# Performance work log

Measured on AMD Instinct MI355X. Metric: run time of the kernel, lower is better.

The kernel has to match this reference:

```python
import jax, jax.numpy as jnp
import numpy as np

EPS = 1e-8
N_CLASSES = 11


def _instance_loss(views_1, views_2, masks, labels):
    # views_*: [1, C, H, W]; masks: [1, K, H, W] binary; labels: [1, K] in [0,11)
    C = views_1.shape[1]
    X1 = views_1[0].reshape(C, -1)                      # [C, P]
    X2 = views_2[0].reshape(C, -1)                      # [C, P]
    K = masks.shape[1]
    M = (masks[0].reshape(K, -1) == 1).astype(X1.dtype) # [K, P]
    lab = labels[0]                                     # [K]

    counts = M.sum(axis=1)                              # [K] pixels per instance
    cnt = jnp.maximum(counts, 1.0)

    # per-instance mean feature vector over masked view-1 pixels
    per_chan_sum = M @ X1.T                             # [K, C]
    means = per_chan_sum / cnt[:, None]                 # [K, C]

    # torch.std over ALL elements of the gathered [N_k, C] block (unbiased)
    n_elem = counts * C                                 # [K]
    sum_all = per_chan_sum.sum(axis=1)                  # [K]
    mean_all = sum_all / jnp.maximum(n_elem, 1.0)
    sumsq = M @ (X1 * X1).sum(axis=0)                   # [K]
    var = (sumsq - n_elem * mean_all * mean_all) / jnp.maximum(n_elem - 1.0, 1.0)
    std = jnp.sqrt(jnp.maximum(var, 0.0))               # [K]

    # pairwise mean cosine sim: sim[i,j] = mean_{p in mask_j} cos(means[i], X2[:,p])
    norm_m = jnp.sqrt((means * means).sum(axis=1))      # [K]
    norm_2 = jnp.sqrt((X2 * X2).sum(axis=0))            # [P]
    D = means @ X2                                      # [K, P]
    ratio = D / jnp.maximum(norm_m[:, None] * norm_2[None, :], EPS)
    sim = (ratio @ M.T) / cnt[None, :]                  # [K, K]

    same = lab[:, None] == lab[None, :]
    eye = jnp.eye(K, dtype=bool)

    instance_sim = jnp.zeros(N_CLASSES, X1.dtype).at[lab].add(jnp.diagonal(sim))
    class_sim = jnp.zeros(N_CLASSES, X1.dtype).at[lab].add(
        jnp.where(same & ~eye, sim, 0.0).sum(axis=1))
    class_std = jnp.zeros(N_CLASSES, X1.dtype).at[lab].add(std)

    # negative-pair buckets: human={1,2}, 4wheel={3..8}, 2wheel={9,10}
    g_hum_4w = (lab >= 1) & (lab <= 8)                  # human or 4wheel
    g_4w_2w = (lab >= 3) & (lab <= 10)                  # 4wheel or 2wheel
    g_hum_2w = ((lab >= 1) & (lab <= 2)) | ((lab >= 9) & (lab <= 10))
    diff = ~same

    def neg_bucket(g):
        pair = diff & g[:, None] & g[None, :]
        c = pair.sum().astype(X1.dtype)
        s = jnp.where(pair, sim, 0.0).sum()
        return jnp.where(c > 1, s / c, s).reshape(1)

    neg_4w_hum = neg_bucket(g_hum_4w)
    neg_4w_2w = neg_bucket(g_4w_2w)
    neg_hum_2w = neg_bucket(g_hum_2w)

    class_counts = jnp.zeros(N_CLASSES, X1.dtype).at[lab].add(1.0)
    many = class_counts > 1
    instance_sim = jnp.where(many, instance_sim / jnp.maximum(class_counts, 1.0), instance_sim)
    class_sim = jnp.where(
        many, class_sim / jnp.maximum(class_counts * (class_counts - 1.0), 1.0), class_sim)
    class_std = jnp.where(many, class_std / jnp.maximum(class_counts, 1.0), class_std)

    return instance_sim, class_sim, neg_4w_hum, neg_4w_2w, neg_hum_2w, class_std


def setup_inputs() -> dict:
    key = jax.random.key(0)
    k1, k2, k3, k4 = jax.random.split(key, 4)
    views_1 = jax.random.normal(k1, (1, 64, 512, 512), dtype=jnp.float32)
    views_2 = jax.random.normal(k2, (1, 64, 512, 512), dtype=jnp.float32)
    masks = jax.random.randint(k3, (1, 16, 512, 512), 0, 2, dtype=jnp.int32)
    labels = jax.random.randint(k4, (1, 16), 0, 11, dtype=jnp.int32)
    return {"views_1": views_1, "views_2": views_2, "masks": masks, "labels": labels}


def reference(views_1, views_2, masks, labels):
    return _instance_loss(views_1, views_2, masks, labels)
```

## Files before the change

kernel.cpp:

```cpp
#include <hip/hip_runtime.h>

#define PIX 262144
#define CCH 64
#define KK  16

typedef __attribute__((ext_vector_type(8))) short short8;
typedef __attribute__((ext_vector_type(4))) float f32x4;

__device__ __forceinline__ float wred64(float v) {
    #pragma unroll
    for (int o = 32; o > 0; o >>= 1) v += __shfl_xor(v, o, 64);
    return v;
}

__global__ __launch_bounds__(256) void k2_all(
        const float* __restrict__ x1, const float* __restrict__ x2,
        const int* __restrict__ masks, float* __restrict__ counts_s,
        float* __restrict__ psum_c, float* __restrict__ psumsq_c,
        float* __restrict__ G_c) {
    __shared__ float gl[4][1024];
    int lane = threadIdx.x & 63;
    int wv   = threadIdx.x >> 6;
    int quad = lane >> 4;
    int n    = lane & 15;
    const short ONE = (short)0x3F80;
    const int* Mrow = masks + (size_t)n * PIX;

    if (blockIdx.x < 1024) {
        int b = blockIdx.x;
        int base = b * 256;
        int cp   = b & 31;
        const float* Xrow = x1 + (size_t)(wv * 16 + n) * PIX;

        f32x4 acc0 = {0.f, 0.f, 0.f, 0.f};
        f32x4 acc1 = {0.f, 0.f, 0.f, 0.f};
        int cnt = 0;

        for (int sc = 0; sc < 2; ++sc) {
            int4 mk[8]; float4 xa[4], xb[4];
            #pragma unroll
            for (int i = 0; i < 4; ++i) {
                int kof = base + sc * 128 + i * 32 + (quad << 3);
                mk[2*i]   = *(const int4*)(Mrow + kof);
                mk[2*i+1] = *(const int4*)(Mrow + kof + 4);
                xa[i] = *(const float4*)(Xrow + kof);
                xb[i] = *(const float4*)(Xrow + kof + 4);
            }
            #pragma unroll
            for (int i = 0; i < 4; ++i) {
                short8 af;
                af[0] = (mk[2*i].x   == 1) ? ONE : (short)0;
                af[1] = (mk[2*i].y   == 1) ? ONE : (short)0;
                af[2] = (mk[2*i].z   == 1) ? ONE : (short)0;
                af[3] = (mk[2*i].w   == 1) ? ONE : (short)0;
                af[4] = (mk[2*i+1].x == 1) ? ONE : (short)0;
                af[5] = (mk[2*i+1].y == 1) ? ONE : (short)0;
                af[6] = (mk[2*i+1].z == 1) ? ONE : (short)0;
                af[7] = (mk[2*i+1].w == 1) ? ONE : (short)0;
                cnt += (mk[2*i].x == 1) + (mk[2*i].y == 1) + (mk[2*i].z == 1) + (mk[2*i].w == 1)
                     + (mk[2*i+1].x == 1) + (mk[2*i+1].y == 1) + (mk[2*i+1].z == 1) + (mk[2*i+1].w == 1);

                float xs[8] = {xa[i].x, xa[i].y, xa[i].z, xa[i].w,
                               xb[i].x, xb[i].y, xb[i].z, xb[i].w};
                short8 bh, bl, qh, ql;
                #pragma unroll
                for (int j = 0; j < 8; ++j) {
                    float v = xs[j];
                    unsigned u = __float_as_uint(v);
                    bh[j] = (short)(u >> 16);
                    float hi = __uint_as_float(u & 0xFFFF0000u);
                    bl[j] = (short)(__float_as_uint(v - hi) >> 16);
                    float sqv = v * v;
                    unsigned uq = __float_as_uint(sqv);
                    qh[j] = (short)(uq >> 16);
                    float hq = __uint_as_float(uq & 0xFFFF0000u);
                    ql[j] = (short)(__float_as_uint(sqv - hq) >> 16);
                }
                acc0 = __builtin_amdgcn_mfma_f32_16x16x32_bf16(af, bh, acc0, 0, 0, 0);
                acc0 = __builtin_amdgcn_mfma_f32_16x16x32_bf16(af, bl, acc0, 0, 0, 0);
                acc1 = __builtin_amdgcn_mfma_f32_16x16x32_bf16(af, qh, acc1, 0, 0, 0);
                acc1 = __builtin_amdgcn_mfma_f32_16x16x32_bf16(af, ql, acc1, 0, 0, 0);
            }
        }

        int col = wv * 16 + n;
        #pragma unroll
        for (int r = 0; r < 4; ++r) {
            int idx = cp * 1024 + (quad * 4 + r) * 64 + col;
            atomicAdd(psum_c + idx, acc0[r]);
            atomicAdd(psumsq_c + idx, acc1[r]);
        }
        if (wv == 0) {
            float fc = (float)cnt;
            fc += __shfl_xor(fc, 16, 64);
            fc += __shfl_xor(fc, 32, 64);
            if (quad == 0) atomicAdd(counts_s + n * 32 + cp, fc);
        }
    } else {
        int b = blockIdx.x - 1024;
        int base = b * 256;
        int cp   = b & 31;

        f32x4 acc[4];
        #pragma unroll
        for (int cg = 0; cg < 4; ++cg) acc[cg] = (f32x4){0.f, 0.f, 0.f, 0.f};

        for (int it = 0; it < 2; ++it) {
            int pxo = base + it * 128 + wv * 32 + (quad << 3);
            int4 mk0 = *(const int4*)(Mrow + pxo);
            int4 mk1 = *(const int4*)(Mrow + pxo + 4);
            float4 xla[4], xlb[4];
            #pragma unroll
            for (int cg = 0; cg < 4; ++cg) {
                const float* Xr = x2 + (size_t)(cg * 16 + n) * PIX;
                xla[cg] = *(const float4*)(Xr + pxo);
                xlb[cg] = *(const float4*)(Xr + pxo + 4);
            }

            float xs[4][8];
            #pragma unroll
            for (int cg = 0; cg < 4; ++cg) {
                xs[cg][0]=xla[cg].x; xs[cg][1]=xla[cg].y; xs[cg][2]=xla[cg].z; xs[cg][3]=xla[cg].w;
                xs[cg][4]=xlb[cg].x; xs[cg][5]=xlb[cg].y; xs[cg][6]=xlb[cg].z; xs[cg][7]=xlb[cg].w;
            }
            float ss[8];
            #pragma unroll
            for (int j = 0; j < 8; ++j) {
                float s = xs[0][j] * xs[0][j];
                s = fmaf(xs[1][j], xs[1][j], s);
                s = fmaf(xs[2][j], xs[2][j], s);
                s = fmaf(xs[3][j], xs[3][j], s);
                ss[j] = s;
            }
            #pragma unroll
            for (int off = 1; off < 16; off <<= 1)
                #pragma unroll
                for (int j = 0; j < 8; ++j)
                    ss[j] += __shfl_xor(ss[j], off, 64);
            float yw[8];
            #pragma unroll
            for (int j = 0; j < 8; ++j)
                yw[j] = (ss[j] > 0.f) ? rsqrtf(ss[j]) : 0.f;

            short8 af;
            af[0] = (mk0.x == 1) ? ONE : (short)0;
            af[1] = (mk0.y == 1) ? ONE : (short)0;
            af[2] = (mk0.z == 1) ? ONE : (short)0;
            af[3] = (mk0.w == 1) ? ONE : (short)0;
            af[4] = (mk1.x == 1) ? ONE : (short)0;
            af[5] = (mk1.y == 1) ? ONE : (short)0;
            af[6] = (mk1.z == 1) ? ONE : (short)0;
            af[7] = (mk1.w == 1) ? ONE : (short)0;

            #pragma unroll
            for (int cg = 0; cg < 4; ++cg) {
                short8 bh, bl;
                #pragma unroll
                for (int j = 0; j < 8; ++j) {
                    float v = xs[cg][j] * yw[j];
                    unsigned u = __float_as_uint(v);
                    bh[j] = (short)(u >> 16);
                    float hi = __uint_as_float(u & 0xFFFF0000u);
                    bl[j] = (short)(__float_as_uint(v - hi) >> 16);
                }
                acc[cg] = __builtin_amdgcn_mfma_f32_16x16x32_bf16(af, bh, acc[cg], 0, 0, 0);
                acc[cg] = __builtin_amdgcn_mfma_f32_16x16x32_bf16(af, bl, acc[cg], 0, 0, 0);
            }
        }

        #pragma unroll
        for (int cg = 0; cg < 4; ++cg)
            #pragma unroll
            for (int r = 0; r < 4; ++r)
                gl[wv][(quad * 4 + r) * 64 + cg * 16 + n] = acc[cg][r];
        __syncthreads();
        for (int e = threadIdx.x; e < 1024; e += 256) {
            float s = gl[0][e] + gl[1][e] + gl[2][e] + gl[3][e];
            atomicAdd(G_c + cp * 1024 + e, s);
        }
    }
}

__global__ __launch_bounds__(256) void k3_finalize(
        const int* __restrict__ labels, const float* __restrict__ counts_s,
        const float* __restrict__ psum_c, const float* __restrict__ psumsq_c,
        const float* __restrict__ G_c, float* __restrict__ out) {
    __shared__ float meansS[16][65];
    __shared__ float Gs[16][65];
    __shared__ float cntS[16], rawcS[16], nmS[16], stdS[16], rowS[16];
    __shared__ float ssq2[16][17];
    __shared__ float ssqS[16];
    __shared__ int   labS[16];
    __shared__ float simS[16][17];
    __shared__ float bred[4][6];
    int t = threadIdx.x;

    if (t < 16) {
        float s = 0.f;
        #pragma unroll 8
        for (int j = 0; j < 32; ++j) s += counts_s[t * 32 + j];
        rawcS[t] = s;
        cntS[t]  = fmaxf(s, 1.f);
        labS[t]  = labels[t];
    }
    {
        int k = t >> 4, seg = t & 15;
        float s = 0.f;
        for (int cp = 0; cp < 32; ++cp) {
            const float4 v = *(const float4*)(psumsq_c + cp * 1024 + k * 64 + seg * 4);
            s += v.x + v.y + v.z + v.w;
        }
        ssq2[k][seg] = s;
    }
    __syncthreads();
    if (t < 16) {
        float s = 0.f;
        #pragma unroll
        for (int seg = 0; seg < 16; ++seg) s += ssq2[t][seg];
        ssqS[t] = s;
    }
    for (int i = t; i < 1024; i += 256) {
        int k = i >> 6, c = i & 63;
        float sp = 0.f, sg = 0.f;
        #pragma unroll 8
        for (int cp = 0; cp < 32; ++cp) {
            sp += psum_c[cp * 1024 + i];
            sg += G_c[cp * 1024 + i];
        }
        meansS[k][c] = sp / cntS[k];
        Gs[k][c] = sg;
    }
    __syncthreads();
    if (t < 16) {
        float s2 = 0.f, sm = 0.f;
        for (int c = 0; c < 64; ++c) {
            float m = meansS[t][c];
            s2 = fmaf(m, m, s2);
            sm += m;
        }
        nmS[t] = sqrtf(s2);
        float ne = rawcS[t] * 64.f;
        float ma = (sm * cntS[t]) / fmaxf(ne, 1.f);
        float var = (ssqS[t] - ne * ma * ma) / fmaxf(ne - 1.f, 1.f);
        stdS[t] = sqrtf(fmaxf(var, 0.f));
    }
    __syncthreads();
    {
        int i = t >> 4, j = t & 15;
        float d = 0.f;
        #pragma unroll 16
        for (int c = 0; c < 64; ++c) d = fmaf(meansS[i][c], Gs[j][c], d);
        simS[i][j] = d / (fmaxf(nmS[i], 1e-30f) * cntS[j]);
    }
    __syncthreads();
    if (t < 16) {
        float s = 0.f;
        int li = labS[t];
        for (int j = 0; j < 16; ++j)
            if (j != t && labS[j] == li) s += simS[t][j];
        rowS[t] = s;
    }
    float s0 = 0.f, s1 = 0.f, s2 = 0.f, c0 = 0.f, c1 = 0.f, c2 = 0.f;
    {
        int i = t >> 4, j = t & 15;
        int li = labS[i], lj = labS[j];
        if (li != lj) {
            float sv = simS[i][j];
            bool gi0 = li >= 1 && li <= 8,  gj0 = lj >= 1 && lj <= 8;
            bool gi1 = li >= 3 && li <= 10, gj1 = lj >= 3 && lj <= 10;
            bool gi2 = (li >= 1 && li <= 2) || (li >= 9 && li <= 10);
            bool gj2 = (lj >= 1 && lj <= 2) || (lj >= 9 && lj <= 10);
            if (gi0 && gj0) { s0 = sv; c0 = 1.f; }
            if (gi1 && gj1) { s1 = sv; c1 = 1.f; }
            if (gi2 && gj2) { s2 = sv; c2 = 1.f; }
        }
    }
    s0 = wred64(s0); s1 = wred64(s1); s2 = wred64(s2);
    c0 = wred64(c0); c1 = wred64(c1); c2 = wred64(c2);
    {
        int wid = t >> 6, lane = t & 63;
        if (lane == 0) {
            bred[wid][0] = s0; bred[wid][1] = s1; bred[wid][2] = s2;
            bred[wid][3] = c0; bred[wid][4] = c1; bred[wid][5] = c2;
        }
    }
    __syncthreads();
    if (t < 11) {
        float cc = 0.f, inst = 0.f, csim = 0.f, cstd = 0.f;
        for (int k = 0; k < 16; ++k) {
            if (labS[k] == t) {
                cc += 1.f;
                inst += simS[k][k];
                csim += rowS[k];
                cstd += stdS[k];
            }
        }
        if (cc > 1.f) {
            inst /= fmaxf(cc, 1.f);
            csim /= fmaxf(cc * (cc - 1.f), 1.f);
            cstd /= cc;
        }
        out[t]      = inst;
        out[11 + t] = csim;
        out[25 + t] = cstd;
    }
    if (t == 0) {
        float S0 = bred[0][0] + bred[1][0] + bred[2][0] + bred[3][0];
        float S1 = bred[0][1] + bred[1][1] + bred[2][1] + bred[3][1];
        float S2 = bred[0][2] + bred[1][2] + bred[2][2] + bred[3][2];
        float C0 = bred[0][3] + bred[1][3] + bred[2][3] + bred[3][3];
        float C1 = bred[0][4] + bred[1][4] + bred[2][4] + bred[3][4];
        float C2 = bred[0][5] + bred[1][5] + bred[2][5] + bred[3][5];
        out[22] = (C0 > 1.f) ? (S0 / C0) : S0;
        out[23] = (C1 > 1.f) ? (S1 / C1) : S1;
        out[24] = (C2 > 1.f) ? (S2 / C2) : S2;
    }
}

extern "C" void kernel_launch(void* const* d_in, const int* in_sizes, int n_in,
                              void* d_out, int out_size, void* d_ws, size_t ws_size,
                              hipStream_t stream) {
    const float* x1     = (const float*)d_in[0];
    const float* x2     = (const float*)d_in[1];
    const int*   masks  = (const int*)d_in[2];
    const int*   labels = (const int*)d_in[3];
    float* out = (float*)d_out;

    float* ws = (float*)d_ws;
    float* counts_s = ws;
    float* psum_c   = counts_s + 512;
    float* psumsq_c = psum_c + 32 * 1024;
    float* G_c      = psumsq_c + 32 * 1024;

    hipMemsetAsync(counts_s, 0, (512 + 3 * 32 * 1024) * sizeof(float), stream);
    k2_all<<<2048, 256, 0, stream>>>(x1, x2, masks, counts_s, psum_c, psumsq_c, G_c);
    k3_finalize<<<1, 256, 0, stream>>>(labels, counts_s, psum_c, psumsq_c, G_c, out);
}
```

Before: 191.1 us.

## Pre-pack masks into 16-bit bitfields and halve per-block pixel work

Adds a pre-pass kernel that packs the 16 int32 instance masks into one 16-bit word per pixel and zeroes the accumulators, replacing the memset. Both halves of the main kernel then read the small packed buffer instead of re-reading the full int32 masks, which cuts global mask traffic. The main grid doubles, with each block covering 128 pixels. The view-2 path drops its shared-memory cross-wave reduction in favour of direct per-wave atomics spread over more partial copies, so global atomic traffic grows considerably.

Result: slower. 225.5 us (+18.0%).

```diff
diff --git a/kernel.cpp b/kernel.cpp
--- a/kernel.cpp
+++ b/kernel.cpp
@@ -3,6 +3,7 @@
 #define PIX 262144
 #define CCH 64
 #define KK  16
+#define ACCF (512 + 3 * 32 * 1024)
 
 typedef __attribute__((ext_vector_type(8))) short short8;
 typedef __attribute__((ext_vector_type(4))) float f32x4;
@@ -13,74 +14,88 @@
     return v;
 }
 
+__global__ __launch_bounds__(256) void k0_pack(
+        const int* __restrict__ masks, unsigned short* __restrict__ packed,
+        float* __restrict__ accz) {
+    int t = blockIdx.x * 256 + threadIdx.x;
+    int p = t * 2;
+    unsigned m0 = 0, m1 = 0;
+    #pragma unroll
+    for (int k = 0; k < KK; ++k) {
+        int2 mv = *(const int2*)(masks + (size_t)k * PIX + p);
+        m0 |= (unsigned)(mv.x == 1) << k;
+        m1 |= (unsigned)(mv.y == 1) << k;
+    }
+    packed[p]     = (unsigned short)m0;
+    packed[p + 1] = (unsigned short)m1;
+    if (t < ACCF) accz[t] = 0.f;
+}
+
 __global__ __launch_bounds__(256) void k2_all(
         const float* __restrict__ x1, const float* __restrict__ x2,
-        const int* __restrict__ masks, float* __restrict__ counts_s,
+        const unsigned short* __restrict__ packed, float* __restrict__ counts_s,
         float* __restrict__ psum_c, float* __restrict__ psumsq_c,
         float* __restrict__ G_c) {
-    __shared__ float gl[4][1024];
     int lane = threadIdx.x & 63;
     int wv   = threadIdx.x >> 6;
     int quad = lane >> 4;
     int n    = lane & 15;
     const short ONE = (short)0x3F80;
-    const int* Mrow = masks + (size_t)n * PIX;
-
-    if (blockIdx.x < 1024) {
+
+    if (blockIdx.x < 2048) {
         int b = blockIdx.x;
-        int base = b * 256;
+        int base = b * 128;
         int cp   = b & 31;
         const float* Xrow = x1 + (size_t)(wv * 16 + n) * PIX;
+
+        int4 pk[4]; float4 xa[4], xb[4];
+        #pragma unroll
+        for (int i = 0; i < 4; ++i) {
+            int kof = base + i * 32 + (quad << 3);
+            pk[i] = *(const int4*)(packed + kof);
+            xa[i] = *(const float4*)(Xrow + kof);
+            xb[i] = *(const float4*)(Xrow + kof + 4);
+        }
 
         f32x4 acc0 = {0.f, 0.f, 0.f, 0.f};
         f32x4 acc1 = {0.f, 0.f, 0.f, 0.f};
         int cnt = 0;
 
-        for (int sc = 0; sc < 2; ++sc) {
-            int4 mk[8]; float4 xa[4], xb[4];
+        #pragma unroll
+        for (int i = 0; i < 4; ++i) {
+            unsigned w0 = (unsigned)pk[i].x, w1 = (unsigned)pk[i].y;
+            unsigned w2 = (unsigned)pk[i].z, w3 = (unsigned)pk[i].w;
+            unsigned b0 = (w0 >> n) & 1u, b1 = (w0 >> (n + 16)) & 1u;
+            unsigned b2 = (w1 >> n) & 1u, b3 = (w1 >> (n + 16)) & 1u;
+            unsigned b4 = (w2 >> n) & 1u, b5 = (w2 >> (n + 16)) & 1u;
+            unsigned b6 = (w3 >> n) & 1u, b7 = (w3 >> (n + 16)) & 1u;
+            short8 af;
+            af[0] = b0 ? ONE : (short)0;  af[1] = b1 ? ONE : (short)0;
+            af[2] = b2 ? ONE : (short)0;  af[3] = b3 ? ONE : (short)0;
+            af[4] = b4 ? ONE : (short)0;  af[5] = b5 ? ONE : (short)0;
+            af[6] = b6 ? ONE : (short)0;  af[7] = b7 ? ONE : (short)0;
+            cnt += (int)(b0 + b1 + b2 + b3 + b4 + b5 + b6 + b7);
+
+            float xs[8] = {xa[i].x, xa[i].y, xa[i].z, xa[i].w,
+                           xb[i].x, xb[i].y, xb[i].z, xb[i].w};
+            short8 bh, bl, qh, ql;
             #pragma unroll
-            for (int i = 0; i < 4; ++i) {
-                int kof = base + sc * 128 + i * 32 + (quad << 3);
-                mk[2*i]   = *(const int4*)(Mrow + kof);
-                mk[2*i+1] = *(const int4*)(Mrow + kof + 4);
-                xa[i] = *(const float4*)(Xrow + kof);
-                xb[i] = *(const float4*)(Xrow + kof + 4);
+            for (int j = 0; j < 8; ++j) {
+                float v = xs[j];
+                unsigned u = __float_as_uint(v);
+                bh[j] = (short)(u >> 16);
+                float hi = __uint_as_float(u & 0xFFFF0000u);
+                bl[j] = (short)(__float_as_uint(v - hi) >> 16);
+                float sqv = v * v;
+                unsigned uq = __float_as_uint(sqv);
+                qh[j] = (short)(uq >> 16);
+                float hq = __uint_as_float(uq & 0xFFFF0000u);
+                ql[j] = (short)(__float_as_uint(sqv - hq) >> 16);
             }
-            #pragma unroll
-            for (int i = 0; i < 4; ++i) {
-                short8 af;
-                af[0] = (mk[2*i].x   == 1) ? ONE : (short)0;
-                af[1] = (mk[2*i].y   == 1) ? ONE : (short)0;
-                af[2] = (mk[2*i].z   == 1) ? ONE : (short)0;
-                af[3] = (mk[2*i].w   == 1) ? ONE : (short)0;
-                af[4] = (mk[2*i+1].x == 1) ? ONE : (short)0;
-                af[5] = (mk[2*i+1].y == 1) ? ONE : (short)0;
-                af[6] = (mk[2*i+1].z == 1) ? ONE : (short)0;
-                af[7] = (mk[2*i+1].w == 1) ? ONE : (short)0;
-                cnt += (mk[2*i].x == 1) + (mk[2*i].y == 1) + (mk[2*i].z == 1) + (mk[2*i].w == 1)
-                     + (mk[2*i+1].x == 1) + (mk[2*i+1].y == 1) + (mk[2*i+1].z == 1) + (mk[2*i+1].w == 1);
-
-                float xs[8] = {xa[i].x, xa[i].y, xa[i].z, xa[i].w,
-                               xb[i].x, xb[i].y, xb[i].z, xb[i].w};
-                short8 bh, bl, qh, ql;
-                #pragma unroll
-                for (int j = 0; j < 8; ++j) {
-                    float v = xs[j];
-                    unsigned u = __float_as_uint(v);
-                    bh[j] = (short)(u >> 16);
-                    float hi = __uint_as_float(u & 0xFFFF0000u);
-                    bl[j] = (short)(__float_as_uint(v - hi) >> 16);
-                    float sqv = v * v;
-                    unsigned uq = __float_as_uint(sqv);
-                    qh[j] = (short)(uq >> 16);
-                    float hq = __uint_as_float(uq & 0xFFFF0000u);
-                    ql[j] = (short)(__float_as_uint(sqv - hq) >> 16);
-                }
-                acc0 = __builtin_amdgcn_mfma_f32_16x16x32_bf16(af, bh, acc0, 0, 0, 0);
-                acc0 = __builtin_amdgcn_mfma_f32_16x16x32_bf16(af, bl, acc0, 0, 0, 0);
-                acc1 = __builtin_amdgcn_mfma_f32_16x16x32_bf16(af, qh, acc1, 0, 0, 0);
-                acc1 = __builtin_amdgcn_mfma_f32_16x16x32_bf16(af, ql, acc1, 0, 0, 0);
-            }
+            acc0 = __builtin_amdgcn_mfma_f32_16x16x32_bf16(af, bh, acc0, 0, 0, 0);
+            acc0 = __builtin_amdgcn_mfma_f32_16x16x32_bf16(af, bl, acc0, 0, 0, 0);
+            acc1 = __builtin_amdgcn_mfma_f32_16x16x32_bf16(af, qh, acc1, 0, 0, 0);
+            acc1 = __builtin_amdgcn_mfma_f32_16x16x32_bf16(af, ql, acc1, 0, 0, 0);
         }
 
         int col = wv * 16 + n;
@@ -97,86 +112,74 @@
             if (quad == 0) atomicAdd(counts_s + n * 32 + cp, fc);
         }
     } else {
-        int b = blockIdx.x - 1024;
-        int base = b * 256;
-        int cp   = b & 31;
-
-        f32x4 acc[4];
-        #pragma unroll
-        for (int cg = 0; cg < 4; ++cg) acc[cg] = (f32x4){0.f, 0.f, 0.f, 0.f};
-
-        for (int it = 0; it < 2; ++it) {
-            int pxo = base + it * 128 + wv * 32 + (quad << 3);
-            int4 mk0 = *(const int4*)(Mrow + pxo);
-            int4 mk1 = *(const int4*)(Mrow + pxo + 4);
-            float4 xla[4], xlb[4];
+        int b = blockIdx.x - 2048;
+        int base = b * 128;
+        int cp   = ((b << 2) + wv) & 31;
+        int pxo  = base + wv * 32 + (quad << 3);
+
+        int4 pk = *(const int4*)(packed + pxo);
+        float4 xla[4], xlb[4];
+        #pragma unroll
+        for (int cg = 0; cg < 4; ++cg) {
+            const float* Xr = x2 + (size_t)(cg * 16 + n) * PIX;
+            xla[cg] = *(const float4*)(Xr + pxo);
+            xlb[cg] = *(const float4*)(Xr + pxo + 4);
+        }
+
+        float xs[4][8];
+        #pragma unroll
+        for (int cg = 0; cg < 4; ++cg) {
+            xs[cg][0]=xla[cg].x; xs[cg][1]=xla[cg].y; xs[cg][2]=xla[cg].z; xs[cg][3]=xla[cg].w;
+            xs[cg][4]=xlb[cg].x; xs[cg][5]=xlb[cg].y; xs[cg][6]=xlb[cg].z; xs[cg][7]=xlb[cg].w;
+        }
+        float ss[8];
+        #pragma unroll
+        for (int j = 0; j < 8; ++j) {
+            float s = xs[0][j] * xs[0][j];
+            s = fmaf(xs[1][j], xs[1][j], s);
+            s = fmaf(xs[2][j], xs[2][j], s);
+            s = fmaf(xs[3][j], xs[3][j], s);
+            ss[j] = s;
+        }
+        #pragma unroll
+        for (int off = 1; off < 16; off <<= 1)
             #pragma unroll
-            for (int cg = 0; cg < 4; ++cg) {
-                const float* Xr = x2 + (size_t)(cg * 16 + n) * PIX;
-                xla[cg] = *(const float4*)(Xr + pxo);
-                xlb[cg] = *(const float4*)(Xr + pxo + 4);
-            }
-
-            float xs[4][8];
-            #pragma unroll
-            for (int cg = 0; cg < 4; ++cg) {
-                xs[cg][0]=xla[cg].x; xs[cg][1]=xla[cg].y; xs[cg][2]=xla[cg].z; xs[cg][3]=xla[cg].w;
-                xs[cg][4]=xlb[cg].x; xs[cg][5]=xlb[cg].y; xs[cg][6]=xlb[cg].z; xs[cg][7]=xlb[cg].w;
-            }
-            float ss[8];
+            for (int j = 0; j < 8; ++j)
+                ss[j] += __shfl_xor(ss[j], off, 64);
+        float yw[8];
+        #pragma unroll
+        for (int j = 0; j < 8; ++j)
+            yw[j] = (ss[j] > 0.f) ? rsqrtf(ss[j]) : 0.f;
+
+        unsigned w0 = (unsigned)pk.x, w1 = (unsigned)pk.y;
+        unsigned w2 = (unsigned)pk.z, w3 = (unsigned)pk.w;
+        short8 af;
+        af[0] = ((w0 >> n) & 1u)        ? ONE : (short)0;
+        af[1] = ((w0 >> (n + 16)) & 1u) ? ONE : (short)0;
+        af[2] = ((w1 >> n) & 1u)        ? ONE : (short)0;
+        af[3] = ((w1 >> (n + 16)) & 1u) ? ONE : (short)0;
+        af[4] = ((w2 >> n) & 1u)        ? ONE : (short)0;
+        af[5] = ((w2 >> (n + 16)) & 1u) ? ONE : (short)0;
+        af[6] = ((w3 >> n) & 1u)        ? ONE : (short)0;
+        af[7] = ((w3 >> (n + 16)) & 1u) ? ONE : (short)0;
+
+        #pragma unroll
+        for (int cg = 0; cg < 4; ++cg) {
+            f32x4 acc = {0.f, 0.f, 0.f, 0.f};
+            short8 bh, bl;
             #pragma unroll
             for (int j = 0; j < 8; ++j) {
-                float s = xs[0][j] * xs[0][j];
-                s = fmaf(xs[1][j], xs[1][j], s);
-                s = fmaf(xs[2][j], xs[2][j], s);
-                s = fmaf(xs[3][j], xs[3][j], s);
-                ss[j] = s;
+                float v = xs[cg][j] * yw[j];
+                unsigned u = __float_as_uint(v);
+                bh[j] = (short)(u >> 16);
+                float hi = __uint_as_float(u & 0xFFFF0000u);
+                bl[j] = (short)(__float_as_uint(v - hi) >> 16);
             }
-            #pragma unroll
-            for (int off = 1; off < 16; off <<= 1)
-                #pragma unroll
-                for (int j = 0; j < 8; ++j)
-                    ss[j] += __shfl_xor(ss[j], off, 64);
-            float yw[8];
-            #pragma unroll
-            for (int j = 0; j < 8; ++j)
-                yw[j] = (ss[j] > 0.f) ? rsqrtf(ss[j]) : 0.f;
-
-            short8 af;
-            af[0] = (mk0.x == 1) ? ONE : (short)0;
-            af[1] = (mk0.y == 1) ? ONE : (short)0;
-            af[2] = (mk0.z == 1) ? ONE : (short)0;
-            af[3] = (mk0.w == 1) ? ONE : (short)0;
-            af[4] = (mk1.x == 1) ? ONE : (short)0;
-            af[5] = (mk1.y == 1) ? ONE : (short)0;
-            af[6] = (mk1.z == 1) ? ONE : (short)0;
-            af[7] = (mk1.w == 1) ? ONE : (short)0;
-
-            #pragma unroll
-            for (int cg = 0; cg < 4; ++cg) {
-                short8 bh, bl;
-                #pragma unroll
-                for (int j = 0; j < 8; ++j) {
-                    float v = xs[cg][j] * yw[j];
-                    unsigned u = __float_as_uint(v);
-                    bh[j] = (short)(u >> 16);
-                    float hi = __uint_as_float(u & 0xFFFF0000u);
-                    bl[j] = (short)(__float_as_uint(v - hi) >> 16);
-                }
-                acc[cg] = __builtin_amdgcn_mfma_f32_16x16x32_bf16(af, bh, acc[cg], 0, 0, 0);
-                acc[cg] = __builtin_amdgcn_mfma_f32_16x16x32_bf16(af, bl, acc[cg], 0, 0, 0);
-            }
-        }
-
-        #pragma unroll
-        for (int cg = 0; cg < 4; ++cg)
+            acc = __builtin_amdgcn_mfma_f32_16x16x32_bf16(af, bh, acc, 0, 0, 0);
+            acc = __builtin_amdgcn_mfma_f32_16x16x32_bf16(af, bl, acc, 0, 0, 0);
             #pragma unroll
             for (int r = 0; r < 4; ++r)
-                gl[wv][(quad * 4 + r) * 64 + cg * 16 + n] = acc[cg][r];
-        __syncthreads();
-        for (int e = threadIdx.x; e < 1024; e += 256) {
-            float s = gl[0][e] + gl[1][e] + gl[2][e] + gl[3][e];
-            atomicAdd(G_c + cp * 1024 + e, s);
+                atomicAdd(G_c + cp * 1024 + (quad * 4 + r) * 64 + cg * 16 + n, acc[r]);
         }
     }
 }
@@ -326,13 +329,15 @@
     const int*   labels = (const int*)d_in[3];
     float* out = (float*)d_out;
 
-    float* ws = (float*)d_ws;
-    float* counts_s = ws;
-    float* psum_c   = counts_s + 512;
+    char* ws = (char*)d_ws;
+    unsigned short* packed = (unsigned short*)ws;
+    float* acc = (float*)(ws + (size_t)PIX * 2);
+    float* counts_s = acc;
+    float* psum_c   = acc + 512;
     float* psumsq_c = psum_c + 32 * 1024;
     float* G_c      = psumsq_c + 32 * 1024;
 
-    hipMemsetAsync(counts_s, 0, (512 + 3 * 32 * 1024) * sizeof(float), stream);
-    k2_all<<<2048, 256, 0, stream>>>(x1, x2, masks, counts_s, psum_c, psumsq_c, G_c);
+    k0_pack<<<512, 256, 0, stream>>>(masks, packed, acc);
+    k2_all<<<4096, 256, 0, stream>>>(x1, x2, packed, counts_s, psum_c, psumsq_c, G_c);
     k3_finalize<<<1, 256, 0, stream>>>(labels, counts_s, psum_c, psumsq_c, G_c, out);
 }
```
